# Kernel tuning notes

Hardware: AMD Instinct MI355X
Metric: run time of the kernel (lower is better)

## Reference

```python
import jax, jax.numpy as jnp
import numpy as np

D_MODEL = 1024
N_HEADS = 16
HEAD_DIM = D_MODEL // N_HEADS


def setup_inputs() -> dict:
    key = jax.random.key(0)
    ks = jax.random.split(key, 5)
    q = jax.random.normal(ks[0], (2, 2048, D_MODEL), dtype=jnp.float32)
    Wq = jax.random.normal(ks[1], (D_MODEL, D_MODEL), dtype=jnp.float32) * (1.0 / np.sqrt(D_MODEL))
    bq = jax.random.normal(ks[2], (D_MODEL,), dtype=jnp.float32) * 0.01
    Wo = jax.random.normal(ks[3], (D_MODEL, D_MODEL), dtype=jnp.float32) * (1.0 / np.sqrt(D_MODEL))
    bo = jax.random.normal(ks[4], (D_MODEL,), dtype=jnp.float32) * 0.01
    return {"q": q, "Wq": Wq, "bq": bq, "Wo": Wo, "bo": bo}


def reference(q, Wq, bq, Wo, bo):
    bs, S, dim = q.shape
    # NOTE: original module (bug-faithfully) projects Q, K and V all with WQ.
    proj = q @ Wq.T + bq  # [B, S, D]
    h = proj.reshape(bs, S, N_HEADS, HEAD_DIM).transpose(0, 2, 1, 3)  # [B, H, S, Dh]
    qh, kh, vh = h, h, h
    scale = HEAD_DIM ** -0.5
    attn = jnp.einsum('bhqd,bhkd->bhqk', qh, kh) * scale  # [B, H, S, S]
    scores = jax.nn.softmax(attn, axis=-1)
    # dropout is identity in inference mode
    vals = jnp.einsum('bhqk,bhkd->bhqd', scores, vh)  # [B, H, S, Dh]
    vals = vals.transpose(0, 2, 1, 3).reshape(bs, S, dim)
    return vals @ Wo.T + bo
```

## Files before the change

kernel.cpp:

```cpp
#include <hip/hip_runtime.h>

#define D_MODEL 1024
#define N_HEADS 16
#define HEAD_DIM 64
#define SEQ 2048
#define BATCH 2
#define M_TOTAL (BATCH*SEQ)

typedef __bf16 bf16;
typedef __bf16 bf16x8 __attribute__((ext_vector_type(8)));
typedef __bf16 bf16x4 __attribute__((ext_vector_type(4)));
typedef float  floatx4 __attribute__((ext_vector_type(4)));

__device__ __forceinline__ void gl2lds16(const bf16* g, bf16* l) {
    __builtin_amdgcn_global_load_lds(
        (const __attribute__((address_space(1))) unsigned int*)g,
        (__attribute__((address_space(3))) unsigned int*)l, 16, 0, 0);
}

__global__ void cvt_all(const float* __restrict__ q, const float* __restrict__ Wq,
                        const float* __restrict__ Wo, bf16* __restrict__ qb,
                        bf16* __restrict__ wqb, bf16* __restrict__ wob) {
    int i = blockIdx.x * 256 + threadIdx.x;
    const float* src; bf16* dst; int off;
    if (i < 1048576)      { src = q;  dst = qb;  off = i; }
    else if (i < 1310720) { src = Wq; dst = wqb; off = i - 1048576; }
    else                  { src = Wo; dst = wob; off = i - 1310720; }
    float4 v = ((const float4*)src)[off];
    bf16x4 o;
    o[0] = (bf16)v.x; o[1] = (bf16)v.y; o[2] = (bf16)v.z; o[3] = (bf16)v.w;
    ((bf16x4*)dst)[off] = o;
}

template<int MODE>
__global__ __launch_bounds__(512)
void gemm_bt_bias_t(const bf16* __restrict__ A, const bf16* __restrict__ B,
                    const float* __restrict__ bias, void* __restrict__ Cout,
                    bf16* __restrict__ Cout2, int M, int N, int K)
{
    __shared__ __align__(16) bf16 smem[16384];
    bf16* As = smem;
    bf16* Bs = smem + 8192;

    const int tid  = threadIdx.x;
    const int lane = tid & 63;
    const int wave = tid >> 6;
    const int quad = lane >> 4;
    const int l16  = lane & 15;
    const int m0   = blockIdx.y * 128;
    const int n0   = blockIdx.x * 128;
    const int wm   = (wave >> 2) * 64;
    const int wn   = (wave & 3) * 32;

    floatx4 acc[4][2];
#pragma unroll
    for (int i = 0; i < 4; i++)
#pragma unroll
        for (int j = 0; j < 2; j++) acc[i][j] = (floatx4){0.f, 0.f, 0.f, 0.f};

    const int srow = tid >> 2;
    const int sc   = (tid & 3) ^ ((srow >> 1) & 3);
    auto issue = [&](int buf, int k0) {
        gl2lds16(A + (size_t)(m0 + srow) * K + k0 + sc * 8, &As[buf * 4096 + tid * 8]);
        gl2lds16(B + (size_t)(n0 + srow) * K + k0 + sc * 8, &Bs[buf * 4096 + tid * 8]);
    };
    issue(0, 0);
    int buf = 0;
    for (int k0 = 0; k0 < K; k0 += 32, buf ^= 1) {
        __syncthreads();
        if (k0 + 32 < K) issue(buf ^ 1, k0 + 32);
        bf16x8 af[4], bfr[2];
#pragma unroll
        for (int i = 0; i < 4; i++) {
            int row = wm + i * 16 + l16;
            af[i] = *(const bf16x8*)&As[buf * 4096 + row * 32 + ((quad ^ ((row >> 1) & 3)) * 8)];
        }
#pragma unroll
        for (int j = 0; j < 2; j++) {
            int row = wn + j * 16 + l16;
            bfr[j] = *(const bf16x8*)&Bs[buf * 4096 + row * 32 + ((quad ^ ((row >> 1) & 3)) * 8)];
        }
#pragma unroll
        for (int i = 0; i < 4; i++)
#pragma unroll
            for (int j = 0; j < 2; j++)
                acc[i][j] = __builtin_amdgcn_mfma_f32_16x16x32_bf16(
                    af[i], bfr[j], acc[i][j], 0, 0, 0);
    }

    if constexpr (MODE == 0) {
        float* C = (float*)Cout;
#pragma unroll
        for (int j = 0; j < 2; j++) {
            int col  = n0 + wn + j * 16 + l16;
            float bv = bias[col];
#pragma unroll
            for (int i = 0; i < 4; i++) {
                int rbase = m0 + wm + i * 16 + quad * 4;
#pragma unroll
                for (int r = 0; r < 4; r++)
                    C[(size_t)(rbase + r) * N + col] = acc[i][j][r] + bv;
            }
        }
    } else {
        bf16* Cb = (bf16*)Cout;
        bf16x4 tile[4][2];
#pragma unroll
        for (int j = 0; j < 2; j++) {
            int col = n0 + wn + j * 16 + l16;
            int h   = col >> 6, d = col & 63;
            float bv = bias[col];
#pragma unroll
            for (int i = 0; i < 4; i++) {
                int rbase = m0 + wm + i * 16 + quad * 4;
                int b  = rbase >> 11;
                int s0 = rbase & 2047;
#pragma unroll
                for (int r = 0; r < 4; r++) {
                    float v = acc[i][j][r] + bv;
                    tile[i][j][r] = (bf16)v;
                    Cb[(((size_t)(b * N_HEADS + h) * SEQ + (s0 + r)) << 6) + d] = (bf16)v;
                }
            }
        }
        __syncthreads();
#pragma unroll
        for (int j = 0; j < 2; j++) {
            int dL = wn + j * 16 + l16;
#pragma unroll
            for (int i = 0; i < 4; i++) {
                int s0 = wm + i * 16 + quad * 4;
                *(bf16x4*)&smem[dL * 128 + (((s0 >> 3) ^ (dL & 15)) * 8) + (s0 & 7)] =
                    tile[i][j];
            }
        }
        __syncthreads();
        {
            int dL   = tid >> 2;
            int hg   = (n0 + dL) >> 6, d = (n0 + dL) & 63;
            int b    = m0 >> 11, sbase = m0 & 2047;
            bf16* dstrow = Cout2 + ((size_t)(b * N_HEADS + hg) * 64 + d) * SEQ + sbase;
#pragma unroll
            for (int cc = 0; cc < 4; cc++) {
                int c    = (tid & 3) * 4 + cc;
                int phys = c ^ (dL & 15);
                *(bf16x8*)(dstrow + c * 8) = *(const bf16x8*)&smem[dL * 128 + phys * 8];
            }
        }
    }
}

__global__ __launch_bounds__(256)
void flash_attn(const bf16* __restrict__ projbf, const bf16* __restrict__ projT,
                bf16* __restrict__ vals)
{
    __shared__ __align__(16) bf16 Ks[2][128 * 64];
    __shared__ __align__(16) bf16 Vt[2][64 * 128];
    __shared__ __align__(16) bf16 Pt[128 * 40];

    const int tid  = threadIdx.x;
    const int lane = tid & 63;
    const int wave = tid >> 6;
    const int quad = lane >> 4;
    const int l16  = lane & 15;
    const int lin  = blockIdx.x;
    const int bh   = (lin & 7) * 4 + (lin >> 7);
    const int q0   = ((lin >> 3) & 15) * 128;
    const bf16* hK  = projbf + (size_t)bh * SEQ * 64;
    const bf16* hVt = projT  + (size_t)bh * 64 * SEQ;
    const int wq0  = wave * 32;

    bf16x8 qf[2][2];
#pragma unroll
    for (int nb = 0; nb < 2; nb++)
#pragma unroll
        for (int ks = 0; ks < 2; ks++)
            qf[nb][ks] = *(const bf16x8*)(hK + (size_t)(q0 + wq0 + nb * 16 + l16) * 64
                                          + ks * 32 + quad * 8);

    floatx4 oacc[4][2];
#pragma unroll
    for (int mb = 0; mb < 4; mb++)
#pragma unroll
        for (int nb = 0; nb < 2; nb++) oacc[mb][nb] = (floatx4){0.f, 0.f, 0.f, 0.f};
    float lsum[2] = {0.f, 0.f};

    auto issue = [&](int buf, int k0) {
#pragma unroll
        for (int it = 0; it < 4; it++) {
            int row = it * 32 + (tid >> 3);
            int c   = (tid & 7) ^ (row & 7);
            gl2lds16(hK + (size_t)(k0 + row) * 64 + c * 8,
                     &Ks[buf][it * 2048 + tid * 8]);
        }
#pragma unroll
        for (int it = 0; it < 4; it++) {
            int row = it * 16 + (tid >> 4);
            int c   = (tid & 15) ^ (row & 15);
            gl2lds16(hVt + (size_t)row * SEQ + k0 + c * 8,
                     &Vt[buf][it * 2048 + tid * 8]);
        }
    };
    issue(0, 0);
    int buf = 0;
    for (int k0 = 0; k0 < SEQ; k0 += 128, buf ^= 1) {
        __syncthreads();
        if (k0 + 128 < SEQ) issue(buf ^ 1, k0 + 128);

#pragma unroll
        for (int ck = 0; ck < 4; ck++) {
#pragma unroll
            for (int kb = 0; kb < 2; kb++) {
                int krow = ck * 32 + kb * 16 + l16;
                bf16x8 kf0 = *(const bf16x8*)&Ks[buf][krow * 64 + ((quad ^ (krow & 7)) * 8)];
                bf16x8 kf1 = *(const bf16x8*)&Ks[buf][krow * 64 + (((4 + quad) ^ (krow & 7)) * 8)];
                floatx4 sacc[2];
#pragma unroll
                for (int nb = 0; nb < 2; nb++) {
                    sacc[nb] = __builtin_amdgcn_mfma_f32_16x16x32_bf16(
                        kf0, qf[nb][0], (floatx4){0.f, 0.f, 0.f, 0.f}, 0, 0, 0);
                    sacc[nb] = __builtin_amdgcn_mfma_f32_16x16x32_bf16(
                        kf1, qf[nb][1], sacc[nb], 0, 0, 0);
                }
#pragma unroll
                for (int nb = 0; nb < 2; nb++) {
                    bf16x4 p4; float ps = 0.f;
#pragma unroll
                    for (int r = 0; r < 4; r++) {
                        float p = __expf(sacc[nb][r] * 0.125f - 16.0f);
                        p4[r] = (bf16)p; ps += p;
                    }
                    lsum[nb] += ps;
                    *(bf16x4*)&Pt[(wq0 + nb * 16 + l16) * 40 + kb * 16 + quad * 4] = p4;
                }
            }
            bf16x8 pf[2];
#pragma unroll
            for (int nb = 0; nb < 2; nb++)
                pf[nb] = *(const bf16x8*)&Pt[(wq0 + nb * 16 + l16) * 40 + quad * 8];
#pragma unroll
            for (int mb = 0; mb < 4; mb++) {
                int vrow = mb * 16 + l16;
                bf16x8 vf = *(const bf16x8*)&Vt[buf][vrow * 128
                                                + (((ck * 4 + quad) ^ (vrow & 15)) * 8)];
#pragma unroll
                for (int nb = 0; nb < 2; nb++)
                    oacc[mb][nb] = __builtin_amdgcn_mfma_f32_16x16x32_bf16(
                        vf, pf[nb], oacc[mb][nb], 0, 0, 0);
            }
        }
    }

#pragma unroll
    for (int nb = 0; nb < 2; nb++) {
        lsum[nb] += __shfl_xor(lsum[nb], 16);
        lsum[nb] += __shfl_xor(lsum[nb], 32);
    }
    const int b = bh >> 4, h = bh & 15;
#pragma unroll
    for (int nb = 0; nb < 2; nb++) {
        float rinv = 1.0f / lsum[nb];
        int q = q0 + wq0 + nb * 16 + l16;
#pragma unroll
        for (int mb = 0; mb < 4; mb++) {
            bf16x4 o4;
#pragma unroll
            for (int r = 0; r < 4; r++) o4[r] = (bf16)(oacc[mb][nb][r] * rinv);
            *(bf16x4*)&vals[((size_t)b * SEQ + q) * D_MODEL + h * 64 + mb * 16 + quad * 4] = o4;
        }
    }
}

extern "C" void kernel_launch(void* const* d_in, const int* in_sizes, int n_in,
                              void* d_out, int out_size, void* d_ws, size_t ws_size,
                              hipStream_t stream)
{
    const float* q  = (const float*)d_in[0];
    const float* Wq = (const float*)d_in[1];
    const float* bq = (const float*)d_in[2];
    const float* Wo = (const float*)d_in[3];
    const float* bo = (const float*)d_in[4];
    float* out = (float*)d_out;

    char* ws = (char*)d_ws;
    bf16* qbf    = (bf16*)(ws);
    bf16* Wqbf   = (bf16*)(ws + (size_t)( 8 << 20));
    bf16* Wobf   = (bf16*)(ws + (size_t)(10 << 20));
    bf16* projbf = (bf16*)(ws + (size_t)(12 << 20));
    bf16* projT  = (bf16*)(ws + (size_t)(20 << 20));
    bf16* valsb  = (bf16*)(ws + (size_t)(28 << 20));

    cvt_all<<<6144, 256, 0, stream>>>(q, Wq, Wo, qbf, Wqbf, Wobf);

    gemm_bt_bias_t<1><<<dim3(8, 32), 512, 0, stream>>>(qbf, Wqbf, bq, (void*)projbf,
                                                       projT, M_TOTAL, D_MODEL, D_MODEL);

    flash_attn<<<512, 256, 0, stream>>>(projbf, projT, valsb);

    gemm_bt_bias_t<0><<<dim3(8, 32), 512, 0, stream>>>(valsb, Wobf, bo, (void*)out,
                                                       nullptr, M_TOTAL, D_MODEL, D_MODEL);
}
```

Baseline: 170.6 us.

## Shrink GEMM tiles to 128x64 with 256 threads and use exp2 in attention

```diff
diff --git a/kernel.cpp b/kernel.cpp
--- a/kernel.cpp
+++ b/kernel.cpp
@@ -33,12 +33,12 @@
 }
 
 template<int MODE>
-__global__ __launch_bounds__(512)
+__global__ __launch_bounds__(256)
 void gemm_bt_bias_t(const bf16* __restrict__ A, const bf16* __restrict__ B,
                     const float* __restrict__ bias, void* __restrict__ Cout,
                     bf16* __restrict__ Cout2, int M, int N, int K)
 {
-    __shared__ __align__(16) bf16 smem[16384];
+    __shared__ __align__(16) bf16 smem[12288];
     bf16* As = smem;
     bf16* Bs = smem + 8192;
 
@@ -48,9 +48,9 @@
     const int quad = lane >> 4;
     const int l16  = lane & 15;
     const int m0   = blockIdx.y * 128;
-    const int n0   = blockIdx.x * 128;
-    const int wm   = (wave >> 2) * 64;
-    const int wn   = (wave & 3) * 32;
+    const int n0   = blockIdx.x * 64;
+    const int wm   = (wave >> 1) * 64;
+    const int wn   = (wave & 1) * 32;
 
     floatx4 acc[4][2];
 #pragma unroll
@@ -59,10 +59,20 @@
         for (int j = 0; j < 2; j++) acc[i][j] = (floatx4){0.f, 0.f, 0.f, 0.f};
 
     const int srow = tid >> 2;
-    const int sc   = (tid & 3) ^ ((srow >> 1) & 3);
+    const int sp   = tid & 3;
     auto issue = [&](int buf, int k0) {
-        gl2lds16(A + (size_t)(m0 + srow) * K + k0 + sc * 8, &As[buf * 4096 + tid * 8]);
-        gl2lds16(B + (size_t)(n0 + srow) * K + k0 + sc * 8, &Bs[buf * 4096 + tid * 8]);
+#pragma unroll
+        for (int it = 0; it < 2; it++) {
+            int row = it * 64 + srow;
+            int c   = sp ^ ((row >> 1) & 3);
+            gl2lds16(A + (size_t)(m0 + row) * K + k0 + c * 8,
+                     &As[buf * 4096 + it * 2048 + tid * 8]);
+        }
+        {
+            int c = sp ^ ((srow >> 1) & 3);
+            gl2lds16(B + (size_t)(n0 + srow) * K + k0 + c * 8,
+                     &Bs[buf * 2048 + tid * 8]);
+        }
     };
     issue(0, 0);
     int buf = 0;
@@ -78,7 +88,7 @@
 #pragma unroll
         for (int j = 0; j < 2; j++) {
             int row = wn + j * 16 + l16;
-            bfr[j] = *(const bf16x8*)&Bs[buf * 4096 + row * 32 + ((quad ^ ((row >> 1) & 3)) * 8)];
+            bfr[j] = *(const bf16x8*)&Bs[buf * 2048 + row * 32 + ((quad ^ ((row >> 1) & 3)) * 8)];
         }
 #pragma unroll
         for (int i = 0; i < 4; i++)
@@ -104,22 +114,22 @@
         }
     } else {
         bf16* Cb = (bf16*)Cout;
+        const int h  = n0 >> 6;
+        const int b  = m0 >> 11;
         bf16x4 tile[4][2];
 #pragma unroll
         for (int j = 0; j < 2; j++) {
-            int col = n0 + wn + j * 16 + l16;
-            int h   = col >> 6, d = col & 63;
-            float bv = bias[col];
+            int dL   = wn + j * 16 + l16;
+            float bv = bias[n0 + dL];
 #pragma unroll
             for (int i = 0; i < 4; i++) {
-                int rbase = m0 + wm + i * 16 + quad * 4;
-                int b  = rbase >> 11;
-                int s0 = rbase & 2047;
+                int sl = wm + i * 16 + quad * 4;
+                int s0 = (m0 & 2047) + sl;
 #pragma unroll
                 for (int r = 0; r < 4; r++) {
                     float v = acc[i][j][r] + bv;
                     tile[i][j][r] = (bf16)v;
-                    Cb[(((size_t)(b * N_HEADS + h) * SEQ + (s0 + r)) << 6) + d] = (bf16)v;
+                    Cb[(((size_t)(b * N_HEADS + h) * SEQ + (s0 + r)) << 6) + dL] = (bf16)v;
                 }
             }
         }
@@ -129,17 +139,16 @@
             int dL = wn + j * 16 + l16;
 #pragma unroll
             for (int i = 0; i < 4; i++) {
-                int s0 = wm + i * 16 + quad * 4;
-                *(bf16x4*)&smem[dL * 128 + (((s0 >> 3) ^ (dL & 15)) * 8) + (s0 & 7)] =
+                int sl = wm + i * 16 + quad * 4;
+                *(bf16x4*)&smem[dL * 128 + (((sl >> 3) ^ (dL & 15)) * 8) + (sl & 7)] =
                     tile[i][j];
             }
         }
         __syncthreads();
         {
-            int dL   = tid >> 2;
-            int hg   = (n0 + dL) >> 6, d = (n0 + dL) & 63;
-            int b    = m0 >> 11, sbase = m0 & 2047;
-            bf16* dstrow = Cout2 + ((size_t)(b * N_HEADS + hg) * 64 + d) * SEQ + sbase;
+            int dL    = tid >> 2;
+            int sbase = m0 & 2047;
+            bf16* dstrow = Cout2 + ((size_t)(b * N_HEADS + h) * 64 + dL) * SEQ + sbase;
 #pragma unroll
             for (int cc = 0; cc < 4; cc++) {
                 int c    = (tid & 3) * 4 + cc;
@@ -227,7 +236,7 @@
                     bf16x4 p4; float ps = 0.f;
 #pragma unroll
                     for (int r = 0; r < 4; r++) {
-                        float p = __expf(sacc[nb][r] * 0.125f - 16.0f);
+                        float p = exp2f(fmaf(sacc[nb][r], 0.18033688f, -23.083120f));
                         p4[r] = (bf16)p; ps += p;
                     }
                     lsum[nb] += ps;
@@ -292,11 +301,11 @@
 
     cvt_all<<<6144, 256, 0, stream>>>(q, Wq, Wo, qbf, Wqbf, Wobf);
 
-    gemm_bt_bias_t<1><<<dim3(8, 32), 512, 0, stream>>>(qbf, Wqbf, bq, (void*)projbf,
-                                                       projT, M_TOTAL, D_MODEL, D_MODEL);
+    gemm_bt_bias_t<1><<<dim3(16, 32), 256, 0, stream>>>(qbf, Wqbf, bq, (void*)projbf,
+                                                        projT, M_TOTAL, D_MODEL, D_MODEL);
 
     flash_attn<<<512, 256, 0, stream>>>(projbf, projT, valsb);
 
-    gemm_bt_bias_t<0><<<dim3(8, 32), 512, 0, stream>>>(valsb, Wobf, bo, (void*)out,
-                                                       nullptr, M_TOTAL, D_MODEL, D_MODEL);
-}
+    gemm_bt_bias_t<0><<<dim3(16, 32), 256, 0, stream>>>(valsb, Wobf, bo, (void*)out,
+                                                        nullptr, M_TOTAL, D_MODEL, D_MODEL);
+}
```

New measurement: 181.5 us. 1.06x slower.
